# Kernel optimization log

Measured on AMD Instinct MI355X. Metric: run time of the kernel, lower is better.

## Reference

```python
import jax, jax.numpy as jnp
import numpy as np

EPS = 1e-5

def _bn_relu(z, gamma, beta):
    # BatchNorm1d (training mode: biased batch stats) + ReLU, per-feature over batch dim
    mean = jnp.mean(z, axis=0)
    var = jnp.var(z, axis=0)  # biased, matches torch BN normalization
    zn = (z - mean) * jax.lax.rsqrt(var + EPS) * gamma + beta
    return jax.nn.relu(zn)


def setup_inputs() -> dict:
    key = jax.random.key(0)
    ks = jax.random.split(key, 16)
    N, D_IN, H, D_OUT = 2097152, 16, 32, 1
    def lin(kw, kb, fan_in, fan_out):
        bound = 1.0 / np.sqrt(fan_in)
        W = jax.random.uniform(kw, (fan_out, fan_in), jnp.float32, -bound, bound)
        b = jax.random.uniform(kb, (fan_out,), jnp.float32, -bound, bound)
        return W, b
    W1, b1 = lin(ks[0], ks[1], D_IN, H)
    W2, b2 = lin(ks[2], ks[3], H, H)
    W3, b3 = lin(ks[4], ks[5], H, H)
    W4, b4 = lin(ks[6], ks[7], H, D_OUT)
    x = jax.random.normal(ks[8], (N, D_IN), jnp.float32)
    return {
        "x": x,
        "W1": W1, "b1": b1, "g1": jnp.ones((H,), jnp.float32), "be1": jnp.zeros((H,), jnp.float32),
        "W2": W2, "b2": b2, "g2": jnp.ones((H,), jnp.float32), "be2": jnp.zeros((H,), jnp.float32),
        "W3": W3, "b3": b3, "g3": jnp.ones((H,), jnp.float32), "be3": jnp.zeros((H,), jnp.float32),
        "W4": W4, "b4": b4,
    }


def reference(x, W1, b1, g1, be1, W2, b2, g2, be2, W3, b3, g3, be3, W4, b4):
    p1 = _bn_relu(x @ W1.T + b1, g1, be1)    # [N, H]
    p2 = _bn_relu(p1 @ W2.T + b2, g2, be2)   # [N, H]
    p3 = _bn_relu(p2 @ W3.T + b3, g3, be3)   # [N, H]
    return p3 @ W4.T + b4                    # [N, 1]
```

## Files before the change

### kernel.cpp

```cpp
#include <hip/hip_runtime.h>

#define EPS 1e-5f
#define NTHR 256
#define NBLK 2048
#define NSLOT 8

typedef __bf16 bf16x8 __attribute__((ext_vector_type(8)));
typedef float f32x16 __attribute__((ext_vector_type(16)));


template<int DEPTH>
__global__ __launch_bounds__(NTHR) void k_fwd(
    const float* __restrict__ x, __bf16* __restrict__ xb,
    const float* __restrict__ W1, const float* __restrict__ b1,
    const float* __restrict__ g1, const float* __restrict__ be1,
    const float* __restrict__ W2, const float* __restrict__ b2,
    const float* __restrict__ g2, const float* __restrict__ be2,
    const float* __restrict__ W3, const float* __restrict__ b3,
    const float* __restrict__ g3, const float* __restrict__ be3,
    const float* __restrict__ W4, const float* __restrict__ b4,
    float* __restrict__ stats, float* __restrict__ out, int N)
{
    constexpr bool STATS = (DEPTH < 4);
    __shared__ float s_stat[3][64];
    __shared__ float s_a[3][32];
    __shared__ float s_e[3][32];
    __shared__ float s_b[64];

    const int tid = threadIdx.x;
    const float invN = 1.0f / (float)N;

    if (tid < 64) {
        for (int L = 0; L < DEPTH - 1; ++L) {
            float a = 0.f;
            #pragma unroll
            for (int s = 0; s < NSLOT; ++s) a += stats[L * (NSLOT * 64) + s * 64 + tid];
            s_stat[L][tid] = a;
        }
    }
    __syncthreads();
    if (tid < 32) {
        const float* gs[3]  = {g1, g2, g3};
        const float* bes[3] = {be1, be2, be3};
        const float* bs[3]  = {b1, b2, b3};
        for (int L = 0; L < DEPTH - 1; ++L) {
            float mu = s_stat[L][tid] * invN;
            float v  = s_stat[L][32 + tid] * invN - mu * mu;
            float a  = gs[L][tid] * rsqrtf(v + EPS);
            s_a[L][tid] = a;
            s_e[L][tid] = bs[L][tid] - mu + bes[L][tid] / a;
        }
    }
    if (STATS && tid < 64) s_b[tid] = 0.f;
    __syncthreads();

    const int lane = tid & 63;
    const int h = lane >> 5;
    const int ml = lane & 31;

    bf16x8 w1f;
    {
        const float* p = W1 + ml * 16 + h * 8;
        #pragma unroll
        for (int j = 0; j < 8; ++j) w1f[j] = (__bf16)p[j];
    }
    bf16x8 w2f0 = {}, w2f1 = {}, w3f0 = {}, w3f1 = {};
    if (DEPTH >= 2) {
        #pragma unroll
        for (int kh = 0; kh < 2; ++kh)
            #pragma unroll
            for (int j = 0; j < 8; ++j) {
                int pk = (j & 3) + 8 * (j >> 2) + 4 * h + 16 * kh;
                float v = W2[ml * 32 + pk] * s_a[0][pk];
                if (kh == 0) w2f0[j] = (__bf16)v; else w2f1[j] = (__bf16)v;
            }
    }
    if (DEPTH >= 3) {
        #pragma unroll
        for (int kh = 0; kh < 2; ++kh)
            #pragma unroll
            for (int j = 0; j < 8; ++j) {
                int pk = (j & 3) + 8 * (j >> 2) + 4 * h + 16 * kh;
                float v = W3[ml * 32 + pk] * s_a[1][pk];
                if (kh == 0) w3f0[j] = (__bf16)v; else w3f1[j] = (__bf16)v;
            }
    }

    f32x16 c1, c2 = {}, c3 = {};
    float w4c[16];
    #pragma unroll
    for (int i = 0; i < 16; ++i) {
        int p = (i & 3) + 8 * (i >> 2) + 4 * h;
        c1[i] = (DEPTH == 1) ? b1[p] : s_e[0][p];
        if (DEPTH >= 2) c2[i] = (DEPTH == 2) ? b2[p] : s_e[1][p];
        if (DEPTH >= 3) c3[i] = (DEPTH == 3) ? b3[p] : s_e[2][p];
        if (DEPTH == 4) w4c[i] = W4[p] * s_a[2][p]; else w4c[i] = 0.f;
    }
    const float b4v = (DEPTH == 4) ? b4[0] : 0.f;

    const int ntiles = N >> 5;
    const int nwaves = NBLK * (NTHR / 64);
    const int gwave  = blockIdx.x * (NTHR / 64) + (tid >> 6);
    const int K      = ntiles / nwaves;

    float sums[16], sqs[16];
    #pragma unroll
    for (int i = 0; i < 16; ++i) { sums[i] = 0.f; sqs[i] = 0.f; }

    auto tile = [&](int t, bf16x8 xf) {
        f32x16 a1 = __builtin_amdgcn_mfma_f32_32x32x16_bf16(w1f, xf, c1, 0, 0, 0);
        if (DEPTH == 1) {
            #pragma unroll
            for (int i = 0; i < 16; ++i) { sums[i] += a1[i]; sqs[i] = fmaf(a1[i], a1[i], sqs[i]); }
            return;
        }
        bf16x8 qa, qb;
        #pragma unroll
        for (int j = 0; j < 8; ++j) {
            qa[j] = (__bf16)fmaxf(a1[j], 0.f);
            qb[j] = (__bf16)fmaxf(a1[8 + j], 0.f);
        }
        f32x16 a2 = __builtin_amdgcn_mfma_f32_32x32x16_bf16(w2f0, qa, c2, 0, 0, 0);
        a2 = __builtin_amdgcn_mfma_f32_32x32x16_bf16(w2f1, qb, a2, 0, 0, 0);
        if (DEPTH == 2) {
            #pragma unroll
            for (int i = 0; i < 16; ++i) { sums[i] += a2[i]; sqs[i] = fmaf(a2[i], a2[i], sqs[i]); }
            return;
        }
        bf16x8 pa, pb;
        #pragma unroll
        for (int j = 0; j < 8; ++j) {
            pa[j] = (__bf16)fmaxf(a2[j], 0.f);
            pb[j] = (__bf16)fmaxf(a2[8 + j], 0.f);
        }
        f32x16 a3 = __builtin_amdgcn_mfma_f32_32x32x16_bf16(w3f0, pa, c3, 0, 0, 0);
        a3 = __builtin_amdgcn_mfma_f32_32x32x16_bf16(w3f1, pb, a3, 0, 0, 0);
        if (DEPTH == 3) {
            #pragma unroll
            for (int i = 0; i < 16; ++i) { sums[i] += a3[i]; sqs[i] = fmaf(a3[i], a3[i], sqs[i]); }
            return;
        }
        float o = 0.f;
        #pragma unroll
        for (int i = 0; i < 16; ++i) o = fmaf(w4c[i], fmaxf(a3[i], 0.f), o);
        o += __shfl_xor(o, 32);
        if (h == 0) out[(t << 5) + ml] = o + b4v;
    };

    if (DEPTH == 1) {
        auto loadraw = [&](int t, float4& u0, float4& u1) {
            const float4* xp = (const float4*)(x + (size_t)((t << 5) + ml) * 16 + h * 8);
            u0 = xp[0]; u1 = xp[1];
        };
        auto cvt = [&](const float4& u0, const float4& u1) -> bf16x8 {
            bf16x8 xf;
            xf[0] = (__bf16)u0.x; xf[1] = (__bf16)u0.y; xf[2] = (__bf16)u0.z; xf[3] = (__bf16)u0.w;
            xf[4] = (__bf16)u1.x; xf[5] = (__bf16)u1.y; xf[6] = (__bf16)u1.z; xf[7] = (__bf16)u1.w;
            return xf;
        };
        float4 a0, a1v, b0, b1v, p0, p1, q0, q1;
        loadraw(gwave, a0, a1v);
        loadraw(gwave + nwaves, b0, b1v);
        for (int i = 0; i < K; i += 2) {
            int t0 = gwave + i * nwaves;
            if (i + 2 < K) {
                loadraw(t0 + 2 * nwaves, p0, p1);
                loadraw(t0 + 3 * nwaves, q0, q1);
            }
            bf16x8 xf0 = cvt(a0, a1v);
            *(bf16x8*)(xb + ((size_t)t0 * 64 + lane) * 8) = xf0;
            bf16x8 xf1 = cvt(b0, b1v);
            *(bf16x8*)(xb + ((size_t)(t0 + nwaves) * 64 + lane) * 8) = xf1;
            tile(t0, xf0);
            tile(t0 + nwaves, xf1);
            a0 = p0; a1v = p1; b0 = q0; b1v = q1;
        }
    } else {
        auto loadxb = [&](int t) -> bf16x8 {
            return *(const bf16x8*)(xb + ((size_t)t * 64 + lane) * 8);
        };
        bf16x8 xa = loadxb(gwave);
        bf16x8 xbv = loadxb(gwave + nwaves);
        for (int i = 0; i < K; i += 2) {
            int t0 = gwave + i * nwaves;
            bf16x8 xc = {}, xd = {};
            if (i + 2 < K) {
                xc = loadxb(t0 + 2 * nwaves);
                xd = loadxb(t0 + 3 * nwaves);
            }
            tile(t0, xa);
            tile(t0 + nwaves, xbv);
            xa = xc; xbv = xd;
        }
    }

    if (STATS) {
        #pragma unroll
        for (int i = 0; i < 16; ++i) {
            float s = sums[i], q = sqs[i];
            #pragma unroll
            for (int d = 1; d <= 16; d <<= 1) {
                s += __shfl_xor(s, d);
                q += __shfl_xor(q, d);
            }
            if (ml == 0) {
                int p = (i & 3) + 8 * (i >> 2) + 4 * h;
                atomicAdd(&s_b[p], s);
                atomicAdd(&s_b[32 + p], q);
            }
        }
        __syncthreads();
        if (tid < 64) {
            int L = DEPTH - 1;
            atomicAdd(&stats[L * (NSLOT * 64) + (blockIdx.x & (NSLOT - 1)) * 64 + tid], s_b[tid]);
        }
    }
}

extern "C" void kernel_launch(void* const* d_in, const int* in_sizes, int n_in,
                              void* d_out, int out_size, void* d_ws, size_t ws_size,
                              hipStream_t stream) {
    const float* x   = (const float*)d_in[0];
    const float* W1  = (const float*)d_in[1];
    const float* b1  = (const float*)d_in[2];
    const float* g1  = (const float*)d_in[3];
    const float* be1 = (const float*)d_in[4];
    const float* W2  = (const float*)d_in[5];
    const float* b2  = (const float*)d_in[6];
    const float* g2  = (const float*)d_in[7];
    const float* be2 = (const float*)d_in[8];
    const float* W3  = (const float*)d_in[9];
    const float* b3  = (const float*)d_in[10];
    const float* g3  = (const float*)d_in[11];
    const float* be3 = (const float*)d_in[12];
    const float* W4  = (const float*)d_in[13];
    const float* b4  = (const float*)d_in[14];
    float* out = (float*)d_out;
    int N = in_sizes[0] / 16;

    __bf16* xb   = (__bf16*)d_ws;
    float* stats = (float*)((char*)d_ws + (size_t)N * 32);

    hipMemsetAsync(stats, 0, 3 * NSLOT * 64 * sizeof(float), stream);

    k_fwd<1><<<NBLK, NTHR, 0, stream>>>(x, xb, W1, b1, g1, be1, W2, b2, g2, be2, W3, b3, g3, be3, W4, b4, stats, out, N);
    k_fwd<2><<<NBLK, NTHR, 0, stream>>>(x, xb, W1, b1, g1, be1, W2, b2, g2, be2, W3, b3, g3, be3, W4, b4, stats, out, N);
    k_fwd<3><<<NBLK, NTHR, 0, stream>>>(x, xb, W1, b1, g1, be1, W2, b2, g2, be2, W3, b3, g3, be3, W4, b4, stats, out, N);
    k_fwd<4><<<NBLK, NTHR, 0, stream>>>(x, xb, W1, b1, g1, be1, W2, b2, g2, be2, W3, b3, g3, be3, W4, b4, stats, out, N);
}
```

Baseline: 345.9 us.

## Interleave two tiles' MFMA chains and deepen xb prefetch with half the blocks

```diff
diff --git a/kernel.cpp b/kernel.cpp
--- a/kernel.cpp
+++ b/kernel.cpp
@@ -2,7 +2,7 @@
 
 #define EPS 1e-5f
 #define NTHR 256
-#define NBLK 2048
+#define NBLK 1024
 #define NSLOT 8
 
 typedef __bf16 bf16x8 __attribute__((ext_vector_type(8)));
@@ -107,42 +107,73 @@
     #pragma unroll
     for (int i = 0; i < 16; ++i) { sums[i] = 0.f; sqs[i] = 0.f; }
 
-    auto tile = [&](int t, bf16x8 xf) {
-        f32x16 a1 = __builtin_amdgcn_mfma_f32_32x32x16_bf16(w1f, xf, c1, 0, 0, 0);
-        if (DEPTH == 1) {
-            #pragma unroll
-            for (int i = 0; i < 16; ++i) { sums[i] += a1[i]; sqs[i] = fmaf(a1[i], a1[i], sqs[i]); }
-            return;
-        }
+    auto accum2 = [&](const f32x16& A, const f32x16& B) {
+        #pragma unroll
+        for (int i = 0; i < 16; ++i) {
+            sums[i] += A[i] + B[i];
+            sqs[i]  = fmaf(A[i], A[i], fmaf(B[i], B[i], sqs[i]));
+        }
+    };
+    auto accum1 = [&](const f32x16& A) {
+        #pragma unroll
+        for (int i = 0; i < 16; ++i) { sums[i] += A[i]; sqs[i] = fmaf(A[i], A[i], sqs[i]); }
+    };
+    auto rp = [&](const f32x16& a, bf16x8& lo, bf16x8& hi) {
+        #pragma unroll
+        for (int j = 0; j < 8; ++j) {
+            lo[j] = (__bf16)fmaxf(a[j], 0.f);
+            hi[j] = (__bf16)fmaxf(a[8 + j], 0.f);
+        }
+    };
+
+    auto pair = [&](int t0, int t1, bf16x8 xf0, bf16x8 xf1) {
+        f32x16 A1 = __builtin_amdgcn_mfma_f32_32x32x16_bf16(w1f, xf0, c1, 0, 0, 0);
+        f32x16 B1 = __builtin_amdgcn_mfma_f32_32x32x16_bf16(w1f, xf1, c1, 0, 0, 0);
+        if (DEPTH == 1) { accum2(A1, B1); return; }
+        bf16x8 qa0, qb0, qa1, qb1;
+        rp(A1, qa0, qb0);
+        rp(B1, qa1, qb1);
+        f32x16 A2 = __builtin_amdgcn_mfma_f32_32x32x16_bf16(w2f0, qa0, c2, 0, 0, 0);
+        f32x16 B2 = __builtin_amdgcn_mfma_f32_32x32x16_bf16(w2f0, qa1, c2, 0, 0, 0);
+        A2 = __builtin_amdgcn_mfma_f32_32x32x16_bf16(w2f1, qb0, A2, 0, 0, 0);
+        B2 = __builtin_amdgcn_mfma_f32_32x32x16_bf16(w2f1, qb1, B2, 0, 0, 0);
+        if (DEPTH == 2) { accum2(A2, B2); return; }
+        rp(A2, qa0, qb0);
+        rp(B2, qa1, qb1);
+        f32x16 A3 = __builtin_amdgcn_mfma_f32_32x32x16_bf16(w3f0, qa0, c3, 0, 0, 0);
+        f32x16 B3 = __builtin_amdgcn_mfma_f32_32x32x16_bf16(w3f0, qa1, c3, 0, 0, 0);
+        A3 = __builtin_amdgcn_mfma_f32_32x32x16_bf16(w3f1, qb0, A3, 0, 0, 0);
+        B3 = __builtin_amdgcn_mfma_f32_32x32x16_bf16(w3f1, qb1, B3, 0, 0, 0);
+        if (DEPTH == 3) { accum2(A3, B3); return; }
+        float oA = 0.f, oB = 0.f;
+        #pragma unroll
+        for (int i = 0; i < 16; ++i) {
+            oA = fmaf(w4c[i], fmaxf(A3[i], 0.f), oA);
+            oB = fmaf(w4c[i], fmaxf(B3[i], 0.f), oB);
+        }
+        oA += __shfl_xor(oA, 32);
+        oB += __shfl_xor(oB, 32);
+        if (h == 0) {
+            out[(t0 << 5) + ml] = oA + b4v;
+            out[(t1 << 5) + ml] = oB + b4v;
+        }
+    };
+
+    auto tile1 = [&](int t, bf16x8 xf) {
+        f32x16 A1 = __builtin_amdgcn_mfma_f32_32x32x16_bf16(w1f, xf, c1, 0, 0, 0);
+        if (DEPTH == 1) { accum1(A1); return; }
         bf16x8 qa, qb;
-        #pragma unroll
-        for (int j = 0; j < 8; ++j) {
-            qa[j] = (__bf16)fmaxf(a1[j], 0.f);
-            qb[j] = (__bf16)fmaxf(a1[8 + j], 0.f);
-        }
-        f32x16 a2 = __builtin_amdgcn_mfma_f32_32x32x16_bf16(w2f0, qa, c2, 0, 0, 0);
-        a2 = __builtin_amdgcn_mfma_f32_32x32x16_bf16(w2f1, qb, a2, 0, 0, 0);
-        if (DEPTH == 2) {
-            #pragma unroll
-            for (int i = 0; i < 16; ++i) { sums[i] += a2[i]; sqs[i] = fmaf(a2[i], a2[i], sqs[i]); }
-            return;
-        }
-        bf16x8 pa, pb;
-        #pragma unroll
-        for (int j = 0; j < 8; ++j) {
-            pa[j] = (__bf16)fmaxf(a2[j], 0.f);
-            pb[j] = (__bf16)fmaxf(a2[8 + j], 0.f);
-        }
-        f32x16 a3 = __builtin_amdgcn_mfma_f32_32x32x16_bf16(w3f0, pa, c3, 0, 0, 0);
-        a3 = __builtin_amdgcn_mfma_f32_32x32x16_bf16(w3f1, pb, a3, 0, 0, 0);
-        if (DEPTH == 3) {
-            #pragma unroll
-            for (int i = 0; i < 16; ++i) { sums[i] += a3[i]; sqs[i] = fmaf(a3[i], a3[i], sqs[i]); }
-            return;
-        }
+        rp(A1, qa, qb);
+        f32x16 A2 = __builtin_amdgcn_mfma_f32_32x32x16_bf16(w2f0, qa, c2, 0, 0, 0);
+        A2 = __builtin_amdgcn_mfma_f32_32x32x16_bf16(w2f1, qb, A2, 0, 0, 0);
+        if (DEPTH == 2) { accum1(A2); return; }
+        rp(A2, qa, qb);
+        f32x16 A3 = __builtin_amdgcn_mfma_f32_32x32x16_bf16(w3f0, qa, c3, 0, 0, 0);
+        A3 = __builtin_amdgcn_mfma_f32_32x32x16_bf16(w3f1, qb, A3, 0, 0, 0);
+        if (DEPTH == 3) { accum1(A3); return; }
         float o = 0.f;
         #pragma unroll
-        for (int i = 0; i < 16; ++i) o = fmaf(w4c[i], fmaxf(a3[i], 0.f), o);
+        for (int i = 0; i < 16; ++i) o = fmaf(w4c[i], fmaxf(A3[i], 0.f), o);
         o += __shfl_xor(o, 32);
         if (h == 0) out[(t << 5) + ml] = o + b4v;
     };
@@ -159,39 +190,49 @@
             return xf;
         };
         float4 a0, a1v, b0, b1v, p0, p1, q0, q1;
-        loadraw(gwave, a0, a1v);
-        loadraw(gwave + nwaves, b0, b1v);
+        int t = gwave;
+        loadraw(t, a0, a1v);
+        loadraw(t + nwaves, b0, b1v);
         for (int i = 0; i < K; i += 2) {
-            int t0 = gwave + i * nwaves;
-            if (i + 2 < K) {
+            int t0 = t + i * nwaves;
+            if (i + 3 < K) {
                 loadraw(t0 + 2 * nwaves, p0, p1);
                 loadraw(t0 + 3 * nwaves, q0, q1);
             }
             bf16x8 xf0 = cvt(a0, a1v);
+            bf16x8 xf1 = cvt(b0, b1v);
             *(bf16x8*)(xb + ((size_t)t0 * 64 + lane) * 8) = xf0;
-            bf16x8 xf1 = cvt(b0, b1v);
             *(bf16x8*)(xb + ((size_t)(t0 + nwaves) * 64 + lane) * 8) = xf1;
-            tile(t0, xf0);
-            tile(t0 + nwaves, xf1);
+            pair(t0, t0 + nwaves, xf0, xf1);
             a0 = p0; a1v = p1; b0 = q0; b1v = q1;
+        }
+        for (int t2 = t + K * nwaves; t2 < ntiles; t2 += nwaves) {
+            float4 u0, u1;
+            loadraw(t2, u0, u1);
+            bf16x8 xf = cvt(u0, u1);
+            *(bf16x8*)(xb + ((size_t)t2 * 64 + lane) * 8) = xf;
+            tile1(t2, xf);
         }
     } else {
         auto loadxb = [&](int t) -> bf16x8 {
             return *(const bf16x8*)(xb + ((size_t)t * 64 + lane) * 8);
         };
-        bf16x8 xa = loadxb(gwave);
-        bf16x8 xbv = loadxb(gwave + nwaves);
+        bf16x8 r0 = loadxb(gwave);
+        bf16x8 r1 = loadxb(gwave + nwaves);
+        bf16x8 r2 = loadxb(gwave + 2 * nwaves);
+        bf16x8 r3 = loadxb(gwave + 3 * nwaves);
         for (int i = 0; i < K; i += 2) {
             int t0 = gwave + i * nwaves;
-            bf16x8 xc = {}, xd = {};
-            if (i + 2 < K) {
-                xc = loadxb(t0 + 2 * nwaves);
-                xd = loadxb(t0 + 3 * nwaves);
-            }
-            tile(t0, xa);
-            tile(t0 + nwaves, xbv);
-            xa = xc; xbv = xd;
-        }
+            bf16x8 n0 = {}, n1 = {};
+            if (i + 5 < K) {
+                n0 = loadxb(t0 + 4 * nwaves);
+                n1 = loadxb(t0 + 5 * nwaves);
+            }
+            pair(t0, t0 + nwaves, r0, r1);
+            r0 = r2; r1 = r3; r2 = n0; r3 = n1;
+        }
+        for (int t2 = gwave + K * nwaves; t2 < ntiles; t2 += nwaves)
+            tile1(t2, loadxb(t2));
     }
 
     if (STATS) {
```

New measurement: 330.1 us. -4.6%, faster.
